# Performance work log

Measured on AMD Instinct MI355X. Metric: run time of the kernel, lower is better.

Reference implementation:

```python
import jax, jax.numpy as jnp
import numpy as np

B, C, H, W = 8, 64, 256, 256
M1, M2 = 16, 16  # half of n_modes=(32,32); rfft last dim keeps n_modes[-1]//2


def setup_inputs() -> dict:
    key = jax.random.key(0)
    ks = jax.random.split(key, 7)
    scale = 1.0 / (C * C)
    return {
        "x": jax.random.normal(ks[0], (B, C, H, W), dtype=jnp.float32),
        "w1r": scale * jax.random.normal(ks[1], (C, C, M1, M2), dtype=jnp.float32),
        "w1i": scale * jax.random.normal(ks[2], (C, C, M1, M2), dtype=jnp.float32),
        "w2r": scale * jax.random.normal(ks[3], (C, C, M1, M2), dtype=jnp.float32),
        "w2i": scale * jax.random.normal(ks[4], (C, C, M1, M2), dtype=jnp.float32),
        "conv_w": jax.random.normal(ks[5], (C, C), dtype=jnp.float32) / np.sqrt(C),
        "conv_b": jax.random.normal(ks[6], (C,), dtype=jnp.float32) * 0.01,
    }


def reference(x, w1r, w1i, w2r, w2i, conv_w, conv_b):
    # ---- SpectralConv branch ----
    # rfft2 over spatial dims with 'ortho' norm: [b, c, H, W//2+1] complex
    x_ft = jnp.fft.rfftn(x, axes=(2, 3), norm="ortho")
    w1 = w1r + 1j * w1i  # positive-frequency corner weights [i, o, m1, m2]
    w2 = w2r + 1j * w2i  # negative-frequency corner weights
    top = jnp.einsum("bixy,ioxy->boxy", x_ft[:, :, :M1, :M2], w1)
    bot = jnp.einsum("bixy,ioxy->boxy", x_ft[:, :, -M1:, :M2], w2)
    out_ft = jnp.zeros((B, C, H, W // 2 + 1), dtype=x_ft.dtype)
    out_ft = out_ft.at[:, :, :M1, :M2].set(top)
    out_ft = out_ft.at[:, :, -M1:, :M2].set(bot)
    x1 = jnp.fft.irfftn(out_ft, s=(H, W), axes=(2, 3), norm="ortho")
    # ---- 1x1 Conv1d residual branch (channel mixing) ----
    x2 = jnp.einsum("oi,bixy->boxy", conv_w, x) + conv_b[None, :, None, None]
    return x1 + x2
```

## Files before the change

### kernel.cpp

```cpp
#include <hip/hip_runtime.h>
#include <math.h>


#define TWOPI_256 0.024543692606170259f
#define INV256    0.00390625f

#define NX   262144
#define NWT  2097152
#define NZ   2097152
#define O_TA  0
#define O_TB  4096
#define O_XR  20480
#define O_XI  (O_XR + NX)
#define O_WTR (O_XI + NX)
#define O_WTI (O_WTR + NWT)
#define O_YR  (O_WTI + NWT)
#define O_YI  (O_YR + NX)
#define O_ZR  (O_YI + NX)
#define O_ZI  (O_ZR + NZ)
#define O_TT  (O_ZI + NZ)
#define O_TD  (O_TT + 4096)

using s16x8 = __attribute__((ext_vector_type(8))) short;
using f32x4 = __attribute__((ext_vector_type(4))) float;

__device__ __forceinline__ unsigned short f2bf(float f) {
    union { float f; unsigned u; } a; a.f = f;
    unsigned r = (a.u + 0x7fffu + ((a.u >> 16) & 1u)) >> 16;
    return (unsigned short)r;
}

__global__ __launch_bounds__(256) void ktabs(unsigned short* __restrict__ tA,
                                             unsigned short* __restrict__ tB,
                                             unsigned short* __restrict__ tD) {
    int idx = blockIdx.x * 256 + threadIdx.x;
    if (idx < 8192) {
        int col = idx >> 8, w = idx & 255;
        int ky = col & 15;
        int mm = (ky * w) & 255;
        float s, c; sincosf((float)mm * TWOPI_256, &s, &c);
        tA[idx] = f2bf(col < 16 ? c * INV256 : -s * INV256);
    } else if (idx < 40960) {
        int j = idx - 8192;
        int kx2 = j >> 9, k = j & 511, h = k >> 1, p = k & 1;
        int kxi = kx2 & 31;
        int kx = (kxi < 16) ? kxi : (224 + kxi);
        int mm = (kx * h) & 255;
        float s, c; sincosf((float)mm * TWOPI_256, &s, &c);
        float v;
        if (kx2 < 32) v = p ? s : c;
        else          v = p ? c : -s;
        tB[j] = f2bf(v);
    } else {
        int j = idx - 40960;
        int ri = j >> 14, rem = j & 16383;
        int h = rem >> 6, k = rem & 63, kxi = k >> 1, p = k & 1;
        int kx = (kxi < 16) ? kxi : (224 + kxi);
        int mm = (kx * h) & 255;
        float s, c; sincosf((float)mm * TWOPI_256, &s, &c);
        float v;
        if (ri == 0) v = p ? -s : c;
        else         v = p ? c : s;
        tD[j] = f2bf(v);
    }
}

__global__ __launch_bounds__(256, 2) void kab_fwd(const float* __restrict__ x,
                                                  const unsigned short* __restrict__ tA,
                                                  const unsigned short* __restrict__ tB,
                                                  float* __restrict__ Xr,
                                                  float* __restrict__ Xi) {
    __shared__ __align__(16) unsigned short xt[16384];
    __shared__ __align__(16) unsigned int   ub[4096];
    const int tid  = threadIdx.x;
    const int bc   = blockIdx.x;
    const int m    = tid & 15;
    const int g    = (tid >> 4) & 3;
    const int wave = tid >> 6;

    const float* xp = x + (size_t)bc * 65536;
    const int hh = tid >> 4;
    const int w4 = tid & 15;

    f32x4 acc[2][4];
#pragma unroll
    for (int a = 0; a < 2; ++a)
#pragma unroll
        for (int fn = 0; fn < 4; ++fn)
#pragma unroll
            for (int r = 0; r < 4; ++r) acc[a][fn][r] = 0.f;

    float4 stg[2][16];
#pragma unroll
    for (int it = 0; it < 16; ++it)
        stg[0][it] = *reinterpret_cast<const float4*>(xp + (it * 16 + hh) * 256 + w4 * 4);

#pragma unroll
    for (int ch = 0; ch < 4; ++ch) {
        const int cur = ch & 1;
        if (ch < 3) {
#pragma unroll
            for (int it = 0; it < 16; ++it)
                stg[cur ^ 1][it] = *reinterpret_cast<const float4*>(
                    xp + (it * 16 + hh) * 256 + (ch + 1) * 64 + w4 * 4);
        }
#pragma unroll
        for (int it = 0; it < 16; ++it) {
            int h = it * 16 + hh;
            float4 v = stg[cur][it];
            unsigned lo = (unsigned)f2bf(v.x) | ((unsigned)f2bf(v.y) << 16);
            unsigned hi = (unsigned)f2bf(v.z) | ((unsigned)f2bf(v.w) << 16);
            int wl  = w4 * 4;
            int blk = (wl >> 3) ^ (h & 7);
            char* p = reinterpret_cast<char*>(xt) + (h << 7) + (blk << 4) + ((wl & 7) << 1);
            *reinterpret_cast<uint2*>(p) = make_uint2(lo, hi);
        }
        __syncthreads();
#pragma unroll
        for (int ks = 0; ks < 2; ++ks) {
            s16x8 a0 = *reinterpret_cast<const s16x8*>(tA + m * 256        + ch * 64 + ks * 32 + 8 * g);
            s16x8 a1 = *reinterpret_cast<const s16x8*>(tA + (16 + m) * 256 + ch * 64 + ks * 32 + 8 * g);
#pragma unroll
            for (int fn = 0; fn < 4; ++fn) {
                int h   = wave * 64 + fn * 16 + m;
                int blk = (4 * ks + g) ^ (h & 7);
                s16x8 bf = *reinterpret_cast<const s16x8*>(
                    reinterpret_cast<const char*>(xt) + (h << 7) + (blk << 4));
                acc[0][fn] = __builtin_amdgcn_mfma_f32_16x16x32_bf16(a0, bf, acc[0][fn], 0, 0, 0);
                acc[1][fn] = __builtin_amdgcn_mfma_f32_16x16x32_bf16(a1, bf, acc[1][fn], 0, 0, 0);
            }
        }
        __syncthreads();
    }

#pragma unroll
    for (int fn = 0; fn < 4; ++fn) {
        int h = wave * 64 + fn * 16 + m;
#pragma unroll
        for (int r = 0; r < 4; ++r) {
            int ky = 4 * g + r;
            unsigned pk = (unsigned)f2bf(acc[0][fn][r]) | ((unsigned)f2bf(acc[1][fn][r]) << 16);
            int blk = (h >> 2) ^ (ky & 7);
            ub[ky * 256 + blk * 4 + (h & 3)] = pk;
        }
    }
    __syncthreads();

    f32x4 acc2;
#pragma unroll
    for (int r = 0; r < 4; ++r) acc2[r] = 0.f;
#pragma unroll
    for (int ks = 0; ks < 16; ++ks) {
        s16x8 a2 = *reinterpret_cast<const s16x8*>(tB + (wave * 16 + m) * 512 + ks * 32 + 8 * g);
        int blk = (4 * ks + g) ^ (m & 7);
        s16x8 b2 = *reinterpret_cast<const s16x8*>(
            reinterpret_cast<const char*>(ub) + m * 1024 + (blk << 4));
        acc2 = __builtin_amdgcn_mfma_f32_16x16x32_bf16(a2, b2, acc2, 0, 0, 0);
    }
#pragma unroll
    for (int r = 0; r < 4; ++r) {
        int kx2 = wave * 16 + 4 * g + r;
        if (kx2 < 32) Xr[(size_t)bc * 512 + kx2 * 16 + m]        = acc2[r];
        else          Xi[(size_t)bc * 512 + (kx2 - 32) * 16 + m] = acc2[r];
    }
}

__global__ __launch_bounds__(256) void kw_prep(const float* __restrict__ w1r,
                                               const float* __restrict__ w1i,
                                               const float* __restrict__ w2r,
                                               const float* __restrict__ w2i,
                                               float* __restrict__ Wtr,
                                               float* __restrict__ Wti) {
    __shared__ float lds[128][65];
    const int tid = threadIdx.x;
    const int a = blockIdx.x >> 6;
    const int i = blockIdx.x & 63;
    const float* src = (a == 0) ? w1r : (a == 1) ? w1i : (a == 2) ? w2r : w2i;
    float* dst = (a & 1) ? Wti : Wtr;
    const int kxoff = (a >> 1) << 4;
    const float* sp = src + (size_t)i * 16384;

    for (int p = 0; p < 2; ++p) {
        if (p) __syncthreads();
#pragma unroll
        for (int it = 0; it < 8; ++it) {
            int f4 = it * 256 + tid;
            int o = f4 >> 5, j4 = f4 & 31;
            float4 v = *reinterpret_cast<const float4*>(sp + o * 256 + p * 128 + j4 * 4);
            lds[j4 * 4 + 0][o] = v.x; lds[j4 * 4 + 1][o] = v.y;
            lds[j4 * 4 + 2][o] = v.z; lds[j4 * 4 + 3][o] = v.w;
        }
        __syncthreads();
        const int o = tid & 63, mq = tid >> 6;
#pragma unroll
        for (int r = 0; r < 32; ++r) {
            int lm = r * 4 + mq;
            int mky = p * 128 + lm;
            int mm = mky >> 4, ky = mky & 15;
            dst[((((size_t)(kxoff + mm)) * 16 + ky) * 64 + i) * 64 + o] = lds[lm][o];
        }
    }
}

__global__ __launch_bounds__(256) void ktrig(unsigned short* __restrict__ ttab) {
    int idx = blockIdx.x * 256 + threadIdx.x;
    int w = idx >> 5, kk = idx & 31, ky = kk >> 1;
    int mm = (ky * w) & 255;
    float s, c;
    sincosf((float)mm * TWOPI_256, &s, &c);
    ttab[idx] = f2bf((kk & 1) ? -s : c);
}

__global__ __launch_bounds__(256) void kc_mix(const float* __restrict__ Xr,
                                              const float* __restrict__ Xi,
                                              const float* __restrict__ Wtr,
                                              const float* __restrict__ Wti,
                                              float* __restrict__ Yr,
                                              float* __restrict__ Yi) {
    __shared__ float xsr[512], xsi[512];
    const int tid = threadIdx.x;
    const int mode = blockIdx.x;
#pragma unroll
    for (int r = 0; r < 2; ++r) {
        int bi = r * 256 + tid;
        xsr[bi] = Xr[(size_t)bi * 512 + mode];
        xsi[bi] = Xi[(size_t)bi * 512 + mode];
    }
    __syncthreads();
    const int o = tid & 63, bg = tid >> 6;
    float yr0 = 0.f, yi0 = 0.f, yr1 = 0.f, yi1 = 0.f;
    const float* wrp = Wtr + (size_t)mode * 4096;
    const float* wip = Wti + (size_t)mode * 4096;
#pragma unroll 8
    for (int i = 0; i < 64; ++i) {
        float wr = wrp[i * 64 + o], wi = wip[i * 64 + o];
        float xr = xsr[bg * 64 + i],        xi = xsi[bg * 64 + i];
        yr0 += xr * wr - xi * wi;  yi0 += xr * wi + xi * wr;
        float xr2 = xsr[(bg + 4) * 64 + i], xi2 = xsi[(bg + 4) * 64 + i];
        yr1 += xr2 * wr - xi2 * wi;  yi1 += xr2 * wi + xi2 * wr;
    }
    const int kxi = mode >> 4, kym = mode & 15;
    const size_t e0 = ((size_t)bg * 64 + o) * 512 + kym * 32 + kxi;
    const size_t e1 = ((size_t)(bg + 4) * 64 + o) * 512 + kym * 32 + kxi;
    Yr[e0] = yr0;  Yi[e0] = yi0;
    Yr[e1] = yr1;  Yi[e1] = yi1;
}

__global__ __launch_bounds__(256) void kd_mfma(const float* __restrict__ Yr2,
                                               const float* __restrict__ Yi2,
                                               const unsigned short* __restrict__ tD,
                                               float* __restrict__ Zr,
                                               float* __restrict__ Zi) {
    __shared__ __align__(16) unsigned short at[4096];
    __shared__ __align__(16) float zt[64][68];
    const int tid = threadIdx.x;
    const int bid = blockIdx.x;
    const int b  = bid >> 7;
    const int og = (bid >> 3) & 15;
    const int ri = (bid >> 2) & 1;
    const int hs = bid & 3;

    {
        const int row = tid >> 2, q = tid & 3;
        const int ol = row >> 4, ky = row & 15;
        const float sc = (ky == 0) ? INV256 : 2.f * INV256;
        const size_t yb = ((size_t)(b * 64 + og * 4 + ol)) * 512 + ky * 32 + q * 8;
        f32x4 r0 = *reinterpret_cast<const f32x4*>(Yr2 + yb);
        f32x4 r1 = *reinterpret_cast<const f32x4*>(Yr2 + yb + 4);
        f32x4 i0 = *reinterpret_cast<const f32x4*>(Yi2 + yb);
        f32x4 i1 = *reinterpret_cast<const f32x4*>(Yi2 + yb + 4);
        unsigned wbuf[8];
#pragma unroll
        for (int t = 0; t < 4; ++t) {
            wbuf[t]     = (unsigned)f2bf(r0[t] * sc) | ((unsigned)f2bf(i0[t] * sc) << 16);
            wbuf[4 + t] = (unsigned)f2bf(r1[t] * sc) | ((unsigned)f2bf(i1[t] * sc) << 16);
        }
        char* base = reinterpret_cast<char*>(at) + row * 128;
        *reinterpret_cast<uint4*>(base + (((2 * q)     ^ (row & 7)) << 4)) = *reinterpret_cast<uint4*>(&wbuf[0]);
        *reinterpret_cast<uint4*>(base + (((2 * q + 1) ^ (row & 7)) << 4)) = *reinterpret_cast<uint4*>(&wbuf[4]);
    }
    __syncthreads();

    const int m = tid & 15, g = (tid >> 4) & 3, wid = tid >> 6;
    const unsigned short* td = tD + ri * 16384;
    const int hg = hs * 64 + wid * 16 + m;

    f32x4 acc[4];
#pragma unroll
    for (int mf = 0; mf < 4; ++mf)
#pragma unroll
        for (int r = 0; r < 4; ++r) acc[mf][r] = 0.f;

#pragma unroll
    for (int ks = 0; ks < 2; ++ks) {
        s16x8 bf = *reinterpret_cast<const s16x8*>(td + hg * 64 + ks * 32 + 8 * g);
#pragma unroll
        for (int mf = 0; mf < 4; ++mf) {
            s16x8 af = *reinterpret_cast<const s16x8*>(
                reinterpret_cast<const char*>(at) + (mf * 16 + m) * 128
                + (((4 * ks + g) ^ (m & 7)) << 4));
            acc[mf] = __builtin_amdgcn_mfma_f32_16x16x32_bf16(af, bf, acc[mf], 0, 0, 0);
        }
    }

#pragma unroll
    for (int mf = 0; mf < 4; ++mf)
#pragma unroll
        for (int r = 0; r < 4; ++r)
            zt[wid * 16 + m][mf * 16 + 4 * g + r] = acc[mf][r];
    __syncthreads();

    float* Zd = ri ? Zi : Zr;
    const int ol = tid >> 6, hloc = (tid >> 2) & 15, kg = tid & 3;
#pragma unroll
    for (int hq = 0; hq < 4; ++hq) {
        f32x4 v = *reinterpret_cast<const f32x4*>(&zt[hq * 16 + hloc][ol * 16 + 4 * kg]);
        size_t off = (((size_t)(b * 64 + og * 4 + ol)) * 256 + hs * 64 + hq * 16 + hloc) * 16 + 4 * kg;
        *reinterpret_cast<f32x4*>(Zd + off) = v;
    }
}

__global__ __launch_bounds__(256) void ke_mfma(const float* __restrict__ x,
                                               const float* __restrict__ Zr,
                                               const float* __restrict__ Zi,
                                               const float* __restrict__ cw,
                                               const float* __restrict__ bias,
                                               const unsigned short* __restrict__ ttab,
                                               float* __restrict__ out) {
    __shared__ unsigned int bsx[4096];
    const int tid = threadIdx.x;
    const int b  = blockIdx.x >> 9;
    const int h  = (blockIdx.x >> 1) & 255;
    const int wh = blockIdx.x & 1;
    const int wbase = wh * 128;

    const size_t xbase = ((size_t)b * 64) * 65536 + (size_t)h * 256 + wbase;
    const int wl4 = (tid & 31) * 4;
    const int ipg = tid >> 5;
    float4 va[4], vb[4];
#pragma unroll
    for (int it = 0; it < 4; ++it) {
        int ip = it * 8 + ipg;
        va[it] = *reinterpret_cast<const float4*>(x + xbase + (size_t)(2 * ip) * 65536 + wl4);
        vb[it] = *reinterpret_cast<const float4*>(x + xbase + (size_t)(2 * ip + 1) * 65536 + wl4);
    }

    const int m = tid & 15;
    const int g = (tid >> 4) & 3;
    const int wave = tid >> 6;
    const int o = wave * 16 + m;

    s16x8 a0, a1, az;
    {
        f32x4 p  = *reinterpret_cast<const f32x4*>(cw + o * 64 + 8 * g);
        f32x4 q  = *reinterpret_cast<const f32x4*>(cw + o * 64 + 8 * g + 4);
        f32x4 p2 = *reinterpret_cast<const f32x4*>(cw + o * 64 + 32 + 8 * g);
        f32x4 q2 = *reinterpret_cast<const f32x4*>(cw + o * 64 + 32 + 8 * g + 4);
        size_t zoff = (((size_t)b * 64 + o) * 256 + h) * 16 + 4 * g;
        f32x4 zr = *reinterpret_cast<const f32x4*>(Zr + zoff);
        f32x4 zi = *reinterpret_cast<const f32x4*>(Zi + zoff);
#pragma unroll
        for (int t = 0; t < 4; ++t) {
            a0[t]     = (short)f2bf(p[t]);  a0[t + 4] = (short)f2bf(q[t]);
            a1[t]     = (short)f2bf(p2[t]); a1[t + 4] = (short)f2bf(q2[t]);
            az[2 * t]     = (short)f2bf(zr[t]);
            az[2 * t + 1] = (short)f2bf(zi[t]);
        }
    }
    s16x8 btr[8];
#pragma unroll
    for (int f = 0; f < 8; ++f) {
        int w = wbase + f * 16 + m;
        btr[f] = *reinterpret_cast<const s16x8*>(ttab + w * 32 + 8 * g);
    }
    f32x4 bv = *reinterpret_cast<const f32x4*>(bias + wave * 16 + 4 * g);

#pragma unroll
    for (int it = 0; it < 4; ++it) {
        int ip = it * 8 + ipg;
        const float* pa = reinterpret_cast<const float*>(&va[it]);
        const float* pb = reinterpret_cast<const float*>(&vb[it]);
#pragma unroll
        for (int j = 0; j < 4; ++j) {
            int wl = wl4 + j;
            int c = (wl ^ (wl >> 3)) & 7;
            unsigned pk = (unsigned)f2bf(pa[j]) | ((unsigned)f2bf(pb[j]) << 16);
            bsx[(wl << 5) + ((((ip >> 2) ^ c) << 2) | (ip & 3))] = pk;
        }
    }
    __syncthreads();

    f32x4 acc[8];
#pragma unroll
    for (int f = 0; f < 8; ++f)
#pragma unroll
        for (int r = 0; r < 4; ++r) acc[f][r] = 0.f;

#pragma unroll
    for (int f = 0; f < 8; ++f) {
        int wl = f * 16 + m;
        int c = (wl ^ (wl >> 3)) & 7;
        const char* rb = reinterpret_cast<const char*>(bsx) + (wl << 7);
        s16x8 bx0 = *reinterpret_cast<const s16x8*>(rb + ((g ^ c) << 4));
        s16x8 bx1 = *reinterpret_cast<const s16x8*>(rb + (((4 + g) ^ c) << 4));
        acc[f] = __builtin_amdgcn_mfma_f32_16x16x32_bf16(a0, bx0, acc[f], 0, 0, 0);
        acc[f] = __builtin_amdgcn_mfma_f32_16x16x32_bf16(a1, bx1, acc[f], 0, 0, 0);
        acc[f] = __builtin_amdgcn_mfma_f32_16x16x32_bf16(az, btr[f], acc[f], 0, 0, 0);
    }

    float* ob = out + ((size_t)(b * 64 + wave * 16 + 4 * g)) * 65536 + (size_t)h * 256 + wbase;
#pragma unroll
    for (int f = 0; f < 8; ++f) {
#pragma unroll
        for (int r = 0; r < 4; ++r)
            ob[(size_t)r * 65536 + f * 16 + m] = acc[f][r] + bv[r];
    }
}

extern "C" void kernel_launch(void* const* d_in, const int* in_sizes, int n_in,
                              void* d_out, int out_size, void* d_ws, size_t ws_size,
                              hipStream_t stream) {
    const float* x   = (const float*)d_in[0];
    const float* w1r = (const float*)d_in[1];
    const float* w1i = (const float*)d_in[2];
    const float* w2r = (const float*)d_in[3];
    const float* w2i = (const float*)d_in[4];
    const float* cw  = (const float*)d_in[5];
    const float* cb  = (const float*)d_in[6];
    float* out = (float*)d_out;
    float* ws  = (float*)d_ws;
    unsigned short* tA   = (unsigned short*)(ws + O_TA);
    unsigned short* tB   = (unsigned short*)(ws + O_TB);
    unsigned short* ttab = (unsigned short*)(ws + O_TT);
    unsigned short* tD   = (unsigned short*)(ws + O_TD);

    ktabs<<<288, 256, 0, stream>>>(tA, tB, tD);
    ktrig<<<32, 256, 0, stream>>>(ttab);
    kw_prep<<<256, 256, 0, stream>>>(w1r, w1i, w2r, w2i, ws + O_WTR, ws + O_WTI);
    kab_fwd<<<512, 256, 0, stream>>>(x, tA, tB, ws + O_XR, ws + O_XI);
    kc_mix<<<512, 256, 0, stream>>>(ws + O_XR, ws + O_XI, ws + O_WTR, ws + O_WTI,
                                    ws + O_YR, ws + O_YI);
    kd_mfma<<<1024, 256, 0, stream>>>(ws + O_YR, ws + O_YI, tD, ws + O_ZR, ws + O_ZI);
    ke_mfma<<<4096, 256, 0, stream>>>(x, ws + O_ZR, ws + O_ZI, cw, cb, ttab, out);
}
```

Measured before the change: 133.1 us.

## Split channel mix over input halves, fuse trig tables, cheaper bf16 packing

The ktrig launch is folded into ktabs, which removes one kernel launch. kc_mix now splits the input-channel reduction into two halves and launches twice as many blocks. Each half writes a partial result to its own buffer, and kd_mfma sums the two partials when it loads them. The round-to-nearest-even f32-to-bf16 conversion is replaced by a simpler round-half-up packing of two values into one word. This cuts ALU work in the hot conversion loops but changes rounding on ties slightly.

```diff
diff --git a/kernel.cpp b/kernel.cpp
--- a/kernel.cpp
+++ b/kernel.cpp
@@ -14,15 +14,18 @@
 #define O_XI  (O_XR + NX)
 #define O_WTR (O_XI + NX)
 #define O_WTI (O_WTR + NWT)
-#define O_YR  (O_WTI + NWT)
-#define O_YI  (O_YR + NX)
-#define O_ZR  (O_YI + NX)
+#define O_YRA (O_WTI + NWT)
+#define O_YIA (O_YRA + NX)
+#define O_ZR  (O_YIA + NX)
 #define O_ZI  (O_ZR + NZ)
 #define O_TT  (O_ZI + NZ)
 #define O_TD  (O_TT + 4096)
+#define O_YRB (O_TD + 16384)
+#define O_YIB (O_YRB + NX)
 
 using s16x8 = __attribute__((ext_vector_type(8))) short;
 using f32x4 = __attribute__((ext_vector_type(4))) float;
+using u32x4 = __attribute__((ext_vector_type(4))) unsigned;
 
 __device__ __forceinline__ unsigned short f2bf(float f) {
     union { float f; unsigned u; } a; a.f = f;
@@ -30,9 +33,15 @@
     return (unsigned short)r;
 }
 
+__device__ __forceinline__ unsigned bfpack(float a, float b) {
+    union { float f; unsigned u; } x, y; x.f = a; y.f = b;
+    return ((x.u + 0x8000u) >> 16) | ((y.u + 0x8000u) & 0xffff0000u);
+}
+
 __global__ __launch_bounds__(256) void ktabs(unsigned short* __restrict__ tA,
                                              unsigned short* __restrict__ tB,
-                                             unsigned short* __restrict__ tD) {
+                                             unsigned short* __restrict__ tD,
+                                             unsigned short* __restrict__ tT) {
     int idx = blockIdx.x * 256 + threadIdx.x;
     if (idx < 8192) {
         int col = idx >> 8, w = idx & 255;
@@ -51,7 +60,7 @@
         if (kx2 < 32) v = p ? s : c;
         else          v = p ? c : -s;
         tB[j] = f2bf(v);
-    } else {
+    } else if (idx < 73728) {
         int j = idx - 40960;
         int ri = j >> 14, rem = j & 16383;
         int h = rem >> 6, k = rem & 63, kxi = k >> 1, p = k & 1;
@@ -62,6 +71,12 @@
         if (ri == 0) v = p ? -s : c;
         else         v = p ? c : s;
         tD[j] = f2bf(v);
+    } else {
+        int j = idx - 73728;
+        int w = j >> 5, kk = j & 31, ky = kk >> 1;
+        int mm = (ky * w) & 255;
+        float s, c; sincosf((float)mm * TWOPI_256, &s, &c);
+        tT[j] = f2bf((kk & 1) ? -s : c);
     }
 }
 
@@ -108,8 +123,8 @@
         for (int it = 0; it < 16; ++it) {
             int h = it * 16 + hh;
             float4 v = stg[cur][it];
-            unsigned lo = (unsigned)f2bf(v.x) | ((unsigned)f2bf(v.y) << 16);
-            unsigned hi = (unsigned)f2bf(v.z) | ((unsigned)f2bf(v.w) << 16);
+            unsigned lo = bfpack(v.x, v.y);
+            unsigned hi = bfpack(v.z, v.w);
             int wl  = w4 * 4;
             int blk = (wl >> 3) ^ (h & 7);
             char* p = reinterpret_cast<char*>(xt) + (h << 7) + (blk << 4) + ((wl & 7) << 1);
@@ -139,7 +154,7 @@
 #pragma unroll
         for (int r = 0; r < 4; ++r) {
             int ky = 4 * g + r;
-            unsigned pk = (unsigned)f2bf(acc[0][fn][r]) | ((unsigned)f2bf(acc[1][fn][r]) << 16);
+            unsigned pk = bfpack(acc[0][fn][r], acc[1][fn][r]);
             int blk = (h >> 2) ^ (ky & 7);
             ub[ky * 256 + blk * 4 + (h & 3)] = pk;
         }
@@ -202,43 +217,38 @@
     }
 }
 
-__global__ __launch_bounds__(256) void ktrig(unsigned short* __restrict__ ttab) {
-    int idx = blockIdx.x * 256 + threadIdx.x;
-    int w = idx >> 5, kk = idx & 31, ky = kk >> 1;
-    int mm = (ky * w) & 255;
-    float s, c;
-    sincosf((float)mm * TWOPI_256, &s, &c);
-    ttab[idx] = f2bf((kk & 1) ? -s : c);
-}
-
 __global__ __launch_bounds__(256) void kc_mix(const float* __restrict__ Xr,
                                               const float* __restrict__ Xi,
                                               const float* __restrict__ Wtr,
                                               const float* __restrict__ Wti,
-                                              float* __restrict__ Yr,
-                                              float* __restrict__ Yi) {
-    __shared__ float xsr[512], xsi[512];
-    const int tid = threadIdx.x;
-    const int mode = blockIdx.x;
-#pragma unroll
-    for (int r = 0; r < 2; ++r) {
-        int bi = r * 256 + tid;
-        xsr[bi] = Xr[(size_t)bi * 512 + mode];
-        xsi[bi] = Xi[(size_t)bi * 512 + mode];
+                                              float* __restrict__ YrA,
+                                              float* __restrict__ YiA,
+                                              float* __restrict__ YrB,
+                                              float* __restrict__ YiB) {
+    __shared__ float xsr[256], xsi[256];
+    const int tid  = threadIdx.x;
+    const int mode = blockIdx.x >> 1;
+    const int ih   = blockIdx.x & 1;
+    {
+        int b = tid >> 5, il = tid & 31;
+        xsr[tid] = Xr[(size_t)(b * 64 + ih * 32 + il) * 512 + mode];
+        xsi[tid] = Xi[(size_t)(b * 64 + ih * 32 + il) * 512 + mode];
     }
     __syncthreads();
     const int o = tid & 63, bg = tid >> 6;
     float yr0 = 0.f, yi0 = 0.f, yr1 = 0.f, yi1 = 0.f;
-    const float* wrp = Wtr + (size_t)mode * 4096;
-    const float* wip = Wti + (size_t)mode * 4096;
+    const float* wrp = Wtr + (size_t)mode * 4096 + ih * 2048;
+    const float* wip = Wti + (size_t)mode * 4096 + ih * 2048;
 #pragma unroll 8
-    for (int i = 0; i < 64; ++i) {
+    for (int i = 0; i < 32; ++i) {
         float wr = wrp[i * 64 + o], wi = wip[i * 64 + o];
-        float xr = xsr[bg * 64 + i],        xi = xsi[bg * 64 + i];
+        float xr = xsr[bg * 32 + i],        xi = xsi[bg * 32 + i];
         yr0 += xr * wr - xi * wi;  yi0 += xr * wi + xi * wr;
-        float xr2 = xsr[(bg + 4) * 64 + i], xi2 = xsi[(bg + 4) * 64 + i];
+        float xr2 = xsr[(bg + 4) * 32 + i], xi2 = xsi[(bg + 4) * 32 + i];
         yr1 += xr2 * wr - xi2 * wi;  yi1 += xr2 * wi + xi2 * wr;
     }
+    float* Yr = ih ? YrB : YrA;
+    float* Yi = ih ? YiB : YiA;
     const int kxi = mode >> 4, kym = mode & 15;
     const size_t e0 = ((size_t)bg * 64 + o) * 512 + kym * 32 + kxi;
     const size_t e1 = ((size_t)(bg + 4) * 64 + o) * 512 + kym * 32 + kxi;
@@ -246,8 +256,10 @@
     Yr[e1] = yr1;  Yi[e1] = yi1;
 }
 
-__global__ __launch_bounds__(256) void kd_mfma(const float* __restrict__ Yr2,
-                                               const float* __restrict__ Yi2,
+__global__ __launch_bounds__(256) void kd_mfma(const float* __restrict__ YrA,
+                                               const float* __restrict__ YiA,
+                                               const float* __restrict__ YrB,
+                                               const float* __restrict__ YiB,
                                                const unsigned short* __restrict__ tD,
                                                float* __restrict__ Zr,
                                                float* __restrict__ Zi) {
@@ -265,15 +277,15 @@
         const int ol = row >> 4, ky = row & 15;
         const float sc = (ky == 0) ? INV256 : 2.f * INV256;
         const size_t yb = ((size_t)(b * 64 + og * 4 + ol)) * 512 + ky * 32 + q * 8;
-        f32x4 r0 = *reinterpret_cast<const f32x4*>(Yr2 + yb);
-        f32x4 r1 = *reinterpret_cast<const f32x4*>(Yr2 + yb + 4);
-        f32x4 i0 = *reinterpret_cast<const f32x4*>(Yi2 + yb);
-        f32x4 i1 = *reinterpret_cast<const f32x4*>(Yi2 + yb + 4);
+        f32x4 r0 = *reinterpret_cast<const f32x4*>(YrA + yb)     + *reinterpret_cast<const f32x4*>(YrB + yb);
+        f32x4 r1 = *reinterpret_cast<const f32x4*>(YrA + yb + 4) + *reinterpret_cast<const f32x4*>(YrB + yb + 4);
+        f32x4 i0 = *reinterpret_cast<const f32x4*>(YiA + yb)     + *reinterpret_cast<const f32x4*>(YiB + yb);
+        f32x4 i1 = *reinterpret_cast<const f32x4*>(YiA + yb + 4) + *reinterpret_cast<const f32x4*>(YiB + yb + 4);
         unsigned wbuf[8];
 #pragma unroll
         for (int t = 0; t < 4; ++t) {
-            wbuf[t]     = (unsigned)f2bf(r0[t] * sc) | ((unsigned)f2bf(i0[t] * sc) << 16);
-            wbuf[4 + t] = (unsigned)f2bf(r1[t] * sc) | ((unsigned)f2bf(i1[t] * sc) << 16);
+            wbuf[t]     = bfpack(r0[t] * sc, i0[t] * sc);
+            wbuf[4 + t] = bfpack(r1[t] * sc, i1[t] * sc);
         }
         char* base = reinterpret_cast<char*>(at) + row * 128;
         *reinterpret_cast<uint4*>(base + (((2 * q)     ^ (row & 7)) << 4)) = *reinterpret_cast<uint4*>(&wbuf[0]);
@@ -359,13 +371,15 @@
         size_t zoff = (((size_t)b * 64 + o) * 256 + h) * 16 + 4 * g;
         f32x4 zr = *reinterpret_cast<const f32x4*>(Zr + zoff);
         f32x4 zi = *reinterpret_cast<const f32x4*>(Zi + zoff);
-#pragma unroll
-        for (int t = 0; t < 4; ++t) {
-            a0[t]     = (short)f2bf(p[t]);  a0[t + 4] = (short)f2bf(q[t]);
-            a1[t]     = (short)f2bf(p2[t]); a1[t + 4] = (short)f2bf(q2[t]);
-            az[2 * t]     = (short)f2bf(zr[t]);
-            az[2 * t + 1] = (short)f2bf(zi[t]);
-        }
+        u32x4 t0 = {bfpack(p[0], p[1]),  bfpack(p[2], p[3]),
+                    bfpack(q[0], q[1]),  bfpack(q[2], q[3])};
+        u32x4 t1 = {bfpack(p2[0], p2[1]), bfpack(p2[2], p2[3]),
+                    bfpack(q2[0], q2[1]), bfpack(q2[2], q2[3])};
+        u32x4 tz = {bfpack(zr[0], zi[0]), bfpack(zr[1], zi[1]),
+                    bfpack(zr[2], zi[2]), bfpack(zr[3], zi[3])};
+        a0 = __builtin_bit_cast(s16x8, t0);
+        a1 = __builtin_bit_cast(s16x8, t1);
+        az = __builtin_bit_cast(s16x8, tz);
     }
     s16x8 btr[8];
 #pragma unroll
@@ -384,7 +398,7 @@
         for (int j = 0; j < 4; ++j) {
             int wl = wl4 + j;
             int c = (wl ^ (wl >> 3)) & 7;
-            unsigned pk = (unsigned)f2bf(pa[j]) | ((unsigned)f2bf(pb[j]) << 16);
+            unsigned pk = bfpack(pa[j], pb[j]);
             bsx[(wl << 5) + ((((ip >> 2) ^ c) << 2) | (ip & 3))] = pk;
         }
     }
@@ -434,12 +448,12 @@
     unsigned short* ttab = (unsigned short*)(ws + O_TT);
     unsigned short* tD   = (unsigned short*)(ws + O_TD);
 
-    ktabs<<<288, 256, 0, stream>>>(tA, tB, tD);
-    ktrig<<<32, 256, 0, stream>>>(ttab);
+    ktabs<<<320, 256, 0, stream>>>(tA, tB, tD, ttab);
     kw_prep<<<256, 256, 0, stream>>>(w1r, w1i, w2r, w2i, ws + O_WTR, ws + O_WTI);
     kab_fwd<<<512, 256, 0, stream>>>(x, tA, tB, ws + O_XR, ws + O_XI);
-    kc_mix<<<512, 256, 0, stream>>>(ws + O_XR, ws + O_XI, ws + O_WTR, ws + O_WTI,
-                                    ws + O_YR, ws + O_YI);
-    kd_mfma<<<1024, 256, 0, stream>>>(ws + O_YR, ws + O_YI, tD, ws + O_ZR, ws + O_ZI);
+    kc_mix<<<1024, 256, 0, stream>>>(ws + O_XR, ws + O_XI, ws + O_WTR, ws + O_WTI,
+                                     ws + O_YRA, ws + O_YIA, ws + O_YRB, ws + O_YIB);
+    kd_mfma<<<1024, 256, 0, stream>>>(ws + O_YRA, ws + O_YIA, ws + O_YRB, ws + O_YIB,
+                                      tD, ws + O_ZR, ws + O_ZI);
     ke_mfma<<<4096, 256, 0, stream>>>(x, ws + O_ZR, ws + O_ZI, cw, cb, ttab, out);
 }
```

Measured after the change: 127.5 us. 1.04x faster.
